# Performance work log

Hardware: AMD Instinct MI355X
Metric: run time of the kernel (lower is better)

The kernel has to match this reference:

```python
import jax, jax.numpy as jnp
import numpy as np

DIM = 1024
HEADS = 16
HEAD_DIM = DIM // HEADS
D_FF = 4 * DIM
EPS = 1e-5


def _layernorm(x, g, b):
    mu = jnp.mean(x, axis=-1, keepdims=True)
    var = jnp.mean(jnp.square(x - mu), axis=-1, keepdims=True)
    return (x - mu) * jax.lax.rsqrt(var + EPS) * g + b


def setup_inputs() -> dict:
    key = jax.random.key(0)
    ks = jax.random.split(key, 8)
    s = 0.02
    return {
        "x": jax.random.normal(ks[0], (2, 2048, DIM), dtype=jnp.float32),
        "Wqkv": jax.random.normal(ks[1], (DIM, 3 * DIM), dtype=jnp.float32) * s,
        "bqkv": jnp.zeros((3 * DIM,), dtype=jnp.float32),
        "Wout": jax.random.normal(ks[2], (DIM, DIM), dtype=jnp.float32) * s,
        "bout": jnp.zeros((DIM,), dtype=jnp.float32),
        "W1": jax.random.normal(ks[3], (DIM, D_FF), dtype=jnp.float32) * s,
        "b1": jnp.zeros((D_FF,), dtype=jnp.float32),
        "W2": jax.random.normal(ks[4], (D_FF, DIM), dtype=jnp.float32) * s,
        "b2": jnp.zeros((DIM,), dtype=jnp.float32),
        "g1": jnp.ones((DIM,), dtype=jnp.float32),
        "be1": jnp.zeros((DIM,), dtype=jnp.float32),
        "g2": jnp.ones((DIM,), dtype=jnp.float32),
        "be2": jnp.zeros((DIM,), dtype=jnp.float32),
    }


def reference(x, Wqkv, bqkv, Wout, bout, W1, b1, W2, b2, g1, be1, g2, be2):
    B, T, C = x.shape
    # --- multi-head self-attention (explicit QK^T softmax, no mask/cache) ---
    qkv = (x @ Wqkv + bqkv).reshape(B, T, 3, HEADS, HEAD_DIM)
    q = qkv[:, :, 0].transpose(0, 2, 1, 3)  # (B,H,T,hd)
    k = qkv[:, :, 1].transpose(0, 2, 1, 3)
    v = qkv[:, :, 2].transpose(0, 2, 1, 3)
    scale = HEAD_DIM ** -0.5
    scores = jnp.einsum("bhqd,bhkd->bhqk", q, k) * scale  # (B,H,T,T)
    attn = jax.nn.softmax(scores, axis=-1)
    o = jnp.einsum("bhqk,bhkd->bhqd", attn, v)
    o = o.transpose(0, 2, 1, 3).reshape(B, T, C)
    attn_out = o @ Wout + bout
    # --- Post-LN: LN applied to sublayer output, then residual ---
    x = x + _layernorm(attn_out, g1, be1)
    # --- FFN with exact GELU ---
    h = jax.nn.gelu(x @ W1 + b1, approximate=False)
    ffn_out = h @ W2 + b2
    x = x + _layernorm(ffn_out, g2, be2)
    return x
```

## Files before the change

### kernel.cpp

```cpp
#include <hip/hip_runtime.h>
#include <cstdint>
#include <cstddef>

#define DIM 1024
#define HEADS 16
#define HD 64
#define DFF 4096
#define TSEQ 2048
#define EPS 1e-5f

#define WAITCNT_VM4 0xF74
#define WAITCNT_VM0 0xF70
#define WAITCNT_VM8 0xF78
#define WAITCNT_VM4_LGKM0 0x074
#define WAITCNT_VM0_LGKM0 0x070

typedef __bf16 bf16x8 __attribute__((ext_vector_type(8)));
typedef float floatx4 __attribute__((ext_vector_type(4)));

__device__ __forceinline__ unsigned short f2bf(float f) {
  union { float f; unsigned int u; } v; v.f = f;
  return (unsigned short)((v.u + 0x7FFFu + ((v.u >> 16) & 1u)) >> 16);
}

__device__ __forceinline__ float gelu_f(float v) {
  const float u = v * (0.7978845608f + 0.0356774081f * v * v);
  const float e = __expf(2.0f * u);
  const float t = 1.0f - 2.0f / (e + 1.0f);
  return 0.5f * v * (1.0f + t);
}

__device__ __forceinline__ void async16(const void* g, void* l) {
  __builtin_amdgcn_global_load_lds(
      (const __attribute__((address_space(1))) void*)g,
      (__attribute__((address_space(3))) void*)l, 16, 0, 0);
}

__global__ __launch_bounds__(256) void prep_all(const float* __restrict__ x,
                                                const float* __restrict__ Wqkv,
                                                const float* __restrict__ Wout,
                                                const float* __restrict__ W1,
                                                const float* __restrict__ W2,
                                                unsigned short* __restrict__ xb,
                                                unsigned short* __restrict__ WqkvT,
                                                unsigned short* __restrict__ WoutT,
                                                unsigned short* __restrict__ W1T,
                                                unsigned short* __restrict__ W2T) {
  const int bid = blockIdx.x;
  const int tid = threadIdx.x;
  if (bid < 4096) {
    const int i = bid * 256 + tid;
    float4 v = ((const float4*)x)[i];
    ushort4 o;
    o.x = f2bf(v.x); o.y = f2bf(v.y); o.z = f2bf(v.z); o.w = f2bf(v.w);
    ((ushort4*)xb)[i] = o;
    return;
  }
  int id = bid - 4096;
  const float* src; unsigned short* dst; int R, C, gx;
  if (id < 3072)      {            src = Wqkv; dst = WqkvT; R = 1024; C = 3072; gx = 96; }
  else if (id < 4096) { id -= 3072; src = Wout; dst = WoutT; R = 1024; C = 1024; gx = 32; }
  else if (id < 8192) { id -= 4096; src = W1;   dst = W1T;   R = 1024; C = 4096; gx = 128; }
  else                { id -= 8192; src = W2;   dst = W2T;   R = 4096; C = 1024; gx = 32; }
  const int c0 = (id % gx) * 32, r0 = (id / gx) * 32;
  const int tx = tid & 31, ty = tid >> 5;
  __shared__ float tile[32][33];
#pragma unroll
  for (int i = 0; i < 32; i += 8)
    tile[ty + i][tx] = src[(size_t)(r0 + ty + i) * C + c0 + tx];
  __syncthreads();
#pragma unroll
  for (int i = 0; i < 32; i += 8)
    dst[(size_t)(c0 + ty + i) * R + r0 + tx] = f2bf(tile[tx][ty + i]);
}

#define PIPELINED_KLOOP(NIT, STRIDE_EXPR)                                           \
  auto issue = [&](int s, int k0) {                                                  \
    async16(Ab0 + k0, &lds[s][tid * 8]);                                             \
    async16(Ab1 + k0, &lds[s][2048 + tid * 8]);                                      \
    async16(Bb0 + k0, &lds[s][4096 + tid * 8]);                                      \
    async16(Bb1 + k0, &lds[s][6144 + tid * 8]);                                      \
  };                                                                                 \
  issue(0, 0);                                                                       \
  issue(1, 32);                                                                      \
  int sidx = 0;                                                                      \
  for (int k = 0; k < (NIT); k++) {                                                  \
    if (k < (NIT)-1) __builtin_amdgcn_s_waitcnt(WAITCNT_VM4);                        \
    else             __builtin_amdgcn_s_waitcnt(WAITCNT_VM0);                        \
    __builtin_amdgcn_s_barrier();                                                    \
    if (k + 2 < (NIT)) {                                                             \
      int s2 = sidx + 2; if (s2 >= 3) s2 -= 3;                                       \
      issue(s2, (k + 2) * 32);                                                       \
    }                                                                                \
    bf16x8 af[4], bg[4];                                                             \
    _Pragma("unroll")                                                                \
    for (int mi = 0; mi < 4; mi++)                                                   \
      af[mi] = *(const bf16x8*)&lds[sidx][(wm + mi * 16 + l16) * 32 + quad * 8];     \
    _Pragma("unroll")                                                                \
    for (int ni = 0; ni < 4; ni++)                                                   \
      bg[ni] = *(const bf16x8*)&lds[sidx][4096 + (wn + ni * 16 + l16) * 32 + quad * 8]; \
    _Pragma("unroll")                                                                \
    for (int mi = 0; mi < 4; mi++)                                                   \
      _Pragma("unroll")                                                              \
      for (int ni = 0; ni < 4; ni++)                                                 \
        acc[mi][ni] =                                                                \
            __builtin_amdgcn_mfma_f32_16x16x32_bf16(af[mi], bg[ni], acc[mi][ni], 0, 0, 0); \
    sidx = (sidx == 2) ? 0 : sidx + 1;                                               \
  }

template <int EPI>
__global__ __launch_bounds__(256) void gemm_bt(const unsigned short* __restrict__ A,
                                               const unsigned short* __restrict__ Bt,
                                               const float* __restrict__ bias,
                                               void* __restrict__ Cout,
                                               int M, int N, int K) {
  __shared__ unsigned short lds[3][8192];
  const int tid = threadIdx.x;
  const int bm = blockIdx.y * 128, bn = blockIdx.x * 128;
  const int wave = tid >> 6, lane = tid & 63;
  const int l16 = lane & 15, quad = lane >> 4;
  const int wm = (wave >> 1) * 64, wn = (wave & 1) * 64;

  floatx4 acc[4][4] = {};

  const int srow = tid >> 2;
  const int scol = (tid & 3) * 8;

  const unsigned short* Ab0 = A + (size_t)(bm + srow) * K + scol;
  const unsigned short* Ab1 = A + (size_t)(bm + 64 + srow) * K + scol;
  const unsigned short* Bb0 = Bt + (size_t)(bn + srow) * K + scol;
  const unsigned short* Bb1 = Bt + (size_t)(bn + 64 + srow) * K + scol;

  const int nit = K >> 5;
  PIPELINED_KLOOP(nit, 32)
  __syncthreads();

  if (EPI == 0) {
#pragma unroll
    for (int ni = 0; ni < 4; ni++) {
      const int col = bn + wn + ni * 16 + l16;
      const float bv = bias[col];
#pragma unroll
      for (int mi = 0; mi < 4; mi++) {
        const int row0 = bm + wm + mi * 16 + quad * 4;
#pragma unroll
        for (int r = 0; r < 4; r++)
          ((float*)Cout)[(size_t)(row0 + r) * N + col] = acc[mi][ni][r] + bv;
      }
    }
  } else {
    unsigned short* eb = &lds[0][wave * 1152];
    float bvv[4];
#pragma unroll
    for (int ni = 0; ni < 4; ni++) bvv[ni] = bias[bn + wn + ni * 16 + l16];
    const int lrow = lane >> 2, ck = lane & 3;
#pragma unroll
    for (int mi = 0; mi < 4; mi++) {
#pragma unroll
      for (int ni = 0; ni < 4; ni++)
#pragma unroll
        for (int r = 0; r < 4; r++)
          eb[(quad * 4 + r) * 72 + ni * 16 + l16] =
              f2bf(gelu_f(acc[mi][ni][r] + bvv[ni]));
      __syncthreads();
      unsigned short* gp =
          (unsigned short*)Cout + (size_t)(bm + wm + mi * 16 + lrow) * N + bn + wn;
#pragma unroll
      for (int j = 0; j < 2; j++)
        *(uint4*)(gp + j * 32 + ck * 8) = *(const uint4*)&eb[lrow * 72 + j * 32 + ck * 8];
      __syncthreads();
    }
  }
}

__global__ __launch_bounds__(256) void gemm_splitk(const unsigned short* __restrict__ A,
                                                   const unsigned short* __restrict__ Bt,
                                                   float* __restrict__ Cp,
                                                   int M, int N, int Ktot, int Ksl) {
  __shared__ unsigned short lds[3][8192];
  const int tid = threadIdx.x;
  const int bm = blockIdx.y * 128, bn = blockIdx.x * 128;
  const int koff = blockIdx.z * Ksl;
  const int wave = tid >> 6, lane = tid & 63;
  const int l16 = lane & 15, quad = lane >> 4;
  const int wm = (wave >> 1) * 64, wn = (wave & 1) * 64;

  floatx4 acc[4][4] = {};

  const int srow = tid >> 2;
  const int scol = (tid & 3) * 8;

  const unsigned short* Ab0 = A + (size_t)(bm + srow) * Ktot + koff + scol;
  const unsigned short* Ab1 = A + (size_t)(bm + 64 + srow) * Ktot + koff + scol;
  const unsigned short* Bb0 = Bt + (size_t)(bn + srow) * Ktot + koff + scol;
  const unsigned short* Bb1 = Bt + (size_t)(bn + 64 + srow) * Ktot + koff + scol;

  const int nit = Ksl >> 5;
  PIPELINED_KLOOP(nit, 32)

  float* out = Cp + (size_t)blockIdx.z * M * (size_t)N;
#pragma unroll
  for (int ni = 0; ni < 4; ni++) {
    const int col = bn + wn + ni * 16 + l16;
#pragma unroll
    for (int mi = 0; mi < 4; mi++) {
      const int row0 = bm + wm + mi * 16 + quad * 4;
#pragma unroll
      for (int r = 0; r < 4; r++)
        out[(size_t)(row0 + r) * N + col] = acc[mi][ni][r];
    }
  }
}

__global__ __launch_bounds__(256) void gemm_qkv(const unsigned short* __restrict__ A,
                                                const unsigned short* __restrict__ Bt,
                                                const float* __restrict__ bias,
                                                unsigned short* __restrict__ Qg,
                                                unsigned short* __restrict__ Kg,
                                                unsigned short* __restrict__ Vtg) {
  const int K = 1024;
  __shared__ unsigned short lds[3][8192];
  const int tid = threadIdx.x;
  const int bm = blockIdx.y * 128, bn = blockIdx.x * 128;
  const int wave = tid >> 6, lane = tid & 63;
  const int l16 = lane & 15, quad = lane >> 4;
  const int wm = (wave >> 1) * 64, wn = (wave & 1) * 64;

  floatx4 acc[4][4] = {};

  const int srow = tid >> 2;
  const int scol = (tid & 3) * 8;

  const unsigned short* Ab0 = A + (size_t)(bm + srow) * K + scol;
  const unsigned short* Ab1 = A + (size_t)(bm + 64 + srow) * K + scol;
  const unsigned short* Bb0 = Bt + (size_t)(bn + srow) * K + scol;
  const unsigned short* Bb1 = Bt + (size_t)(bn + 64 + srow) * K + scol;

  const int nit = K >> 5;
  PIPELINED_KLOOP(nit, 32)

#pragma unroll
  for (int ni = 0; ni < 4; ni++) {
    const int col = bn + wn + ni * 16 + l16;
    const float bv = bias[col];
    const int sec = col >> 10;
    const int cc = col & 1023;
    const int hh = cc >> 6, dd = cc & 63;
#pragma unroll
    for (int mi = 0; mi < 4; mi++) {
      const int row0 = bm + wm + mi * 16 + quad * 4;
      const int b2 = row0 >> 11, tt0 = row0 & 2047;
      if (sec == 0) {
        unsigned short* q = Qg + ((size_t)(b2 * HEADS + hh) * TSEQ + tt0) * HD + dd;
#pragma unroll
        for (int r = 0; r < 4; r++)
          q[(size_t)r * HD] = f2bf((acc[mi][ni][r] + bv) * 0.125f);
      } else if (sec == 1) {
        unsigned short* k = Kg + ((size_t)(b2 * HEADS + hh) * TSEQ + tt0) * HD + dd;
#pragma unroll
        for (int r = 0; r < 4; r++)
          k[(size_t)r * HD] = f2bf(acc[mi][ni][r] + bv);
      } else {
        ushort4 o;
        o.x = f2bf(acc[mi][ni][0] + bv);
        o.y = f2bf(acc[mi][ni][1] + bv);
        o.z = f2bf(acc[mi][ni][2] + bv);
        o.w = f2bf(acc[mi][ni][3] + bv);
        *(ushort4*)(Vtg + ((size_t)(b2 * HEADS + hh) * HD + dd) * TSEQ + tt0) = o;
      }
    }
  }
}

__global__ __launch_bounds__(256) void attn_mfma(const unsigned short* __restrict__ Qg,
                                                 const unsigned short* __restrict__ Kg,
                                                 const unsigned short* __restrict__ Vtg,
                                                 unsigned short* __restrict__ ob) {
  __shared__ unsigned short QPs[128 * 64];
  __shared__ unsigned short Ks[3][64 * 64];
  __shared__ unsigned short Vs[3][64 * 64];
  const int qt = blockIdx.x, h = blockIdx.y, b = blockIdx.z;
  const int tid = threadIdx.x;
  const int w = tid >> 6, lane = tid & 63, l16 = lane & 15, quad = lane >> 4;

  const int r0 = tid >> 3;
  const int c0 = (tid & 7) ^ (r0 & 7);

  const char* Qbase = (const char*)(Qg + ((size_t)(b * HEADS + h) * TSEQ + qt * 128) * HD);
  const char* Kbase = (const char*)(Kg + (size_t)(b * HEADS + h) * TSEQ * HD);
  const char* Vbase = (const char*)(Vtg + (size_t)(b * HEADS + h) * HD * TSEQ);

  auto issueKV = [&](int s, int ch) {
    const size_t koff = (size_t)ch * 64;
#pragma unroll
    for (int i = 0; i < 2; i++) {
      async16(Kbase + (koff + r0 + i * 32) * 128 + c0 * 16,
              (char*)Ks[s] + (i * 256 + tid) * 16);
      async16(Vbase + (size_t)(r0 + i * 32) * (TSEQ * 2) + koff * 2 + c0 * 16,
              (char*)Vs[s] + (i * 256 + tid) * 16);
    }
  };

#pragma unroll
  for (int i = 0; i < 4; i++)
    async16(Qbase + (size_t)(r0 + i * 32) * 128 + c0 * 16, (char*)QPs + (i * 256 + tid) * 16);
  issueKV(0, 0);
  issueKV(1, 1);

  __builtin_amdgcn_s_waitcnt(WAITCNT_VM8);
  __builtin_amdgcn_s_barrier();

  bf16x8 qf[2][2];
#pragma unroll
  for (int mi = 0; mi < 2; mi++)
#pragma unroll
    for (int kt = 0; kt < 2; kt++) {
      const int row = w * 32 + mi * 16 + l16;
      qf[mi][kt] = *(const bf16x8*)((const char*)QPs + row * 128 +
                                    (((quad + 4 * kt) ^ (row & 7)) * 16));
    }

  union { unsigned short u[8]; bf16x8 b; } onesu;
#pragma unroll
  for (int j = 0; j < 8; j++) onesu.u[j] = 0x3F80;
  const bf16x8 ones = onesu.b;

  floatx4 oacc[2][5] = {};
  char* Pw = (char*)QPs + w * 4096;

  const int NC = TSEQ / 64;
  int sidx = 0;
  for (int ch = 0; ch < NC; ch++) {
    if (ch < NC - 1) __builtin_amdgcn_s_waitcnt(WAITCNT_VM4_LGKM0);
    else             __builtin_amdgcn_s_waitcnt(WAITCNT_VM0_LGKM0);
    __builtin_amdgcn_s_barrier();
    if (ch + 2 < NC) {
      int s2 = sidx + 2; if (s2 >= 3) s2 -= 3;
      issueKV(s2, ch + 2);
    }
    floatx4 sacc[2][4] = {};
#pragma unroll
    for (int kt = 0; kt < 2; kt++) {
#pragma unroll
      for (int ni = 0; ni < 4; ni++) {
        const int row = ni * 16 + l16;
        bf16x8 kf = *(const bf16x8*)((const char*)Ks[sidx] + row * 128 +
                                     (((quad + 4 * kt) ^ (row & 7)) * 16));
#pragma unroll
        for (int mi = 0; mi < 2; mi++)
          sacc[mi][ni] =
              __builtin_amdgcn_mfma_f32_16x16x32_bf16(qf[mi][kt], kf, sacc[mi][ni], 0, 0, 0);
      }
    }
#pragma unroll
    for (int mi = 0; mi < 2; mi++)
#pragma unroll
      for (int ni = 0; ni < 4; ni++)
#pragma unroll
        for (int r = 0; r < 4; r++) {
          const float p = __expf(sacc[mi][ni][r]);
          const unsigned int pu = __builtin_bit_cast(unsigned int, p);
          const int m = mi * 16 + quad * 4 + r;
          const int key = ni * 16 + l16;
          *((unsigned short*)(Pw + m * 128 + (((key >> 3) ^ (m & 7)) * 16) +
                              (key & 7) * 2)) = (unsigned short)(pu >> 16);
        }
#pragma unroll
    for (int kt = 0; kt < 2; kt++) {
      bf16x8 pf[2], vf[4];
#pragma unroll
      for (int mi = 0; mi < 2; mi++) {
        const int row = mi * 16 + l16;
        pf[mi] = *(const bf16x8*)(Pw + row * 128 + (((quad + 4 * kt) ^ (row & 7)) * 16));
      }
#pragma unroll
      for (int nj = 0; nj < 4; nj++) {
        const int vrow = nj * 16 + l16;
        vf[nj] = *(const bf16x8*)((const char*)Vs[sidx] + vrow * 128 +
                                  (((quad + 4 * kt) ^ (vrow & 7)) * 16));
      }
#pragma unroll
      for (int mi = 0; mi < 2; mi++) {
#pragma unroll
        for (int nj = 0; nj < 4; nj++)
          oacc[mi][nj] =
              __builtin_amdgcn_mfma_f32_16x16x32_bf16(pf[mi], vf[nj], oacc[mi][nj], 0, 0, 0);
        oacc[mi][4] =
            __builtin_amdgcn_mfma_f32_16x16x32_bf16(pf[mi], ones, oacc[mi][4], 0, 0, 0);
      }
    }
    sidx = (sidx == 2) ? 0 : sidx + 1;
  }

#pragma unroll
  for (int mi = 0; mi < 2; mi++)
#pragma unroll
    for (int r = 0; r < 4; r++) {
      const float inv = 1.0f / oacc[mi][4][r];
      const int t = qt * 128 + w * 32 + mi * 16 + quad * 4 + r;
      unsigned short* orow = ob + (size_t)(b * TSEQ + t) * DIM + h * HD + l16;
#pragma unroll
      for (int nj = 0; nj < 4; nj++)
        orow[nj * 16] = f2bf(oacc[mi][nj][r] * inv);
    }
}

template <int NP, int WBF>
__global__ __launch_bounds__(256) void add_ln_red(const float* __restrict__ xin,
                                                  const float* __restrict__ parts,
                                                  const float* __restrict__ bias,
                                                  const float* __restrict__ gw,
                                                  const float* __restrict__ bw,
                                                  float* __restrict__ xout,
                                                  unsigned short* __restrict__ xbf) {
  const size_t MN = (size_t)4096 * DIM;
  const int row = blockIdx.x;
  const int tid = threadIdx.x;
  const int c = tid * 4;
  const size_t base = (size_t)row * DIM;
  float4 v = *(const float4*)(parts + base + c);
#pragma unroll
  for (int p = 1; p < NP; p++) {
    float4 t = *(const float4*)(parts + p * MN + base + c);
    v.x += t.x; v.y += t.y; v.z += t.z; v.w += t.w;
  }
  float4 bb = *(const float4*)(bias + c);
  v.x += bb.x; v.y += bb.y; v.z += bb.z; v.w += bb.w;

  float s = v.x + v.y + v.z + v.w;
  float s2 = v.x * v.x + v.y * v.y + v.z * v.z + v.w * v.w;
#pragma unroll
  for (int off = 1; off < 64; off <<= 1) {
    s += __shfl_xor(s, off);
    s2 += __shfl_xor(s2, off);
  }
  __shared__ float rsum[4], rsq[4];
  if ((tid & 63) == 0) { rsum[tid >> 6] = s; rsq[tid >> 6] = s2; }
  __syncthreads();
  s = rsum[0] + rsum[1] + rsum[2] + rsum[3];
  s2 = rsq[0] + rsq[1] + rsq[2] + rsq[3];
  const float mu = s * (1.0f / DIM);
  const float var = s2 * (1.0f / DIM) - mu * mu;
  const float rstd = rsqrtf(var + EPS);
  float4 xv = *(const float4*)(xin + base + c);
  float4 gv = *(const float4*)(gw + c);
  float4 bv = *(const float4*)(bw + c);
  float4 o;
  o.x = xv.x + (v.x - mu) * rstd * gv.x + bv.x;
  o.y = xv.y + (v.y - mu) * rstd * gv.y + bv.y;
  o.z = xv.z + (v.z - mu) * rstd * gv.z + bv.z;
  o.w = xv.w + (v.w - mu) * rstd * gv.w + bv.w;
  *(float4*)(xout + base + c) = o;
  if (WBF) {
    ushort4 ob;
    ob.x = f2bf(o.x); ob.y = f2bf(o.y); ob.z = f2bf(o.z); ob.w = f2bf(o.w);
    *(ushort4*)(xbf + base + c) = ob;
  }
}

extern "C" void kernel_launch(void* const* d_in, const int* in_sizes, int n_in,
                              void* d_out, int out_size, void* d_ws, size_t ws_size,
                              hipStream_t stream) {
  const float* x    = (const float*)d_in[0];
  const float* Wqkv = (const float*)d_in[1];
  const float* bqkv = (const float*)d_in[2];
  const float* Wout = (const float*)d_in[3];
  const float* bout = (const float*)d_in[4];
  const float* W1   = (const float*)d_in[5];
  const float* b1   = (const float*)d_in[6];
  const float* W2   = (const float*)d_in[7];
  const float* b2   = (const float*)d_in[8];
  const float* g1   = (const float*)d_in[9];
  const float* be1  = (const float*)d_in[10];
  const float* g2   = (const float*)d_in[11];
  const float* be2  = (const float*)d_in[12];

  char* w = (char*)d_ws;
  const size_t MB = 1048576;
  unsigned short* xb     = (unsigned short*)(w + 0 * MB);
  unsigned short* WqkvT  = (unsigned short*)(w + 8 * MB);
  unsigned short* WoutT  = (unsigned short*)(w + 14 * MB);
  unsigned short* W1T    = (unsigned short*)(w + 16 * MB);
  unsigned short* W2T    = (unsigned short*)(w + 24 * MB);
  unsigned short* Qb     = (unsigned short*)(w + 32 * MB);
  unsigned short* Kb     = (unsigned short*)(w + 40 * MB);
  unsigned short* Vtb    = (unsigned short*)(w + 48 * MB);
  unsigned short* obuf   = (unsigned short*)(w + 64 * MB);
  float*          atno_p = (float*)(w + 72 * MB);
  float*          x1     = (float*)(w + 104 * MB);
  unsigned short* x1b    = (unsigned short*)(w + 120 * MB);
  unsigned short* hb     = (unsigned short*)(w + 128 * MB);
  float*          ffn_p  = (float*)(w + 32 * MB);

  prep_all<<<16384, 256, 0, stream>>>(x, Wqkv, Wout, W1, W2, xb, WqkvT, WoutT, W1T, W2T);

  gemm_qkv<<<dim3(24, 32), 256, 0, stream>>>(xb, WqkvT, bqkv, Qb, Kb, Vtb);
  attn_mfma<<<dim3(16, 16, 2), 256, 0, stream>>>(Qb, Kb, Vtb, obuf);
  gemm_splitk<<<dim3(8, 32, 2), 256, 0, stream>>>(obuf, WoutT, atno_p, 4096, 1024, 1024, 512);
  add_ln_red<2, 1><<<4096, 256, 0, stream>>>(x, atno_p, bout, g1, be1, x1, x1b);
  gemm_bt<1><<<dim3(32, 32), 256, 0, stream>>>(x1b, W1T, b1, hb, 4096, 4096, 1024);
  gemm_splitk<<<dim3(8, 32, 2), 256, 0, stream>>>(hb, W2T, ffn_p, 4096, 1024, 4096, 2048);
  add_ln_red<2, 0><<<4096, 256, 0, stream>>>(x1, ffn_p, b2, g2, be2, (float*)d_out, nullptr);
}
```

Baseline: 364.4 us.

## Split attention key range in two halves and add combine kernel

```diff
diff --git a/kernel.cpp b/kernel.cpp
--- a/kernel.cpp
+++ b/kernel.cpp
@@ -11,8 +11,6 @@
 
 #define WAITCNT_VM4 0xF74
 #define WAITCNT_VM0 0xF70
-#define WAITCNT_VM8 0xF78
-#define WAITCNT_VM4_LGKM0 0x074
 #define WAITCNT_VM0_LGKM0 0x070
 
 typedef __bf16 bf16x8 __attribute__((ext_vector_type(8)));
@@ -21,6 +19,14 @@
 __device__ __forceinline__ unsigned short f2bf(float f) {
   union { float f; unsigned int u; } v; v.f = f;
   return (unsigned short)((v.u + 0x7FFFu + ((v.u >> 16) & 1u)) >> 16);
+}
+
+__device__ __forceinline__ float fast_exp2(float x) {
+#if __has_builtin(__builtin_amdgcn_exp2f)
+  return __builtin_amdgcn_exp2f(x);
+#else
+  return exp2f(x);
+#endif
 }
 
 __device__ __forceinline__ float gelu_f(float v) {
@@ -254,7 +260,7 @@
         unsigned short* q = Qg + ((size_t)(b2 * HEADS + hh) * TSEQ + tt0) * HD + dd;
 #pragma unroll
         for (int r = 0; r < 4; r++)
-          q[(size_t)r * HD] = f2bf((acc[mi][ni][r] + bv) * 0.125f);
+          q[(size_t)r * HD] = f2bf((acc[mi][ni][r] + bv) * 0.1803368867f);
       } else if (sec == 1) {
         unsigned short* k = Kg + ((size_t)(b2 * HEADS + hh) * TSEQ + tt0) * HD + dd;
 #pragma unroll
@@ -275,11 +281,15 @@
 __global__ __launch_bounds__(256) void attn_mfma(const unsigned short* __restrict__ Qg,
                                                  const unsigned short* __restrict__ Kg,
                                                  const unsigned short* __restrict__ Vtg,
-                                                 unsigned short* __restrict__ ob) {
+                                                 float* __restrict__ Op,
+                                                 float* __restrict__ Lp) {
   __shared__ unsigned short QPs[128 * 64];
-  __shared__ unsigned short Ks[3][64 * 64];
-  __shared__ unsigned short Vs[3][64 * 64];
-  const int qt = blockIdx.x, h = blockIdx.y, b = blockIdx.z;
+  __shared__ unsigned short Ks[2][64 * 64];
+  __shared__ unsigned short Vs[2][64 * 64];
+  const int idx = blockIdx.x;
+  const int bh2 = idx & 63, qt = idx >> 6;
+  const int half = bh2 & 1, bh = bh2 >> 1;
+  const int h = bh & 15, b = bh >> 4;
   const int tid = threadIdx.x;
   const int w = tid >> 6, lane = tid & 63, l16 = lane & 15, quad = lane >> 4;
 
@@ -287,8 +297,10 @@
   const int c0 = (tid & 7) ^ (r0 & 7);
 
   const char* Qbase = (const char*)(Qg + ((size_t)(b * HEADS + h) * TSEQ + qt * 128) * HD);
-  const char* Kbase = (const char*)(Kg + (size_t)(b * HEADS + h) * TSEQ * HD);
-  const char* Vbase = (const char*)(Vtg + (size_t)(b * HEADS + h) * HD * TSEQ);
+  const char* Kbase = (const char*)(Kg + (size_t)(b * HEADS + h) * TSEQ * HD) +
+                      (size_t)half * 1024 * 128;
+  const char* Vbase = (const char*)(Vtg + (size_t)(b * HEADS + h) * HD * TSEQ) +
+                      (size_t)half * 2048;
 
   auto issueKV = [&](int s, int ch) {
     const size_t koff = (size_t)ch * 64;
@@ -305,9 +317,8 @@
   for (int i = 0; i < 4; i++)
     async16(Qbase + (size_t)(r0 + i * 32) * 128 + c0 * 16, (char*)QPs + (i * 256 + tid) * 16);
   issueKV(0, 0);
-  issueKV(1, 1);
-
-  __builtin_amdgcn_s_waitcnt(WAITCNT_VM8);
+
+  __builtin_amdgcn_s_waitcnt(WAITCNT_VM4);
   __builtin_amdgcn_s_barrier();
 
   bf16x8 qf[2][2];
@@ -328,23 +339,19 @@
   floatx4 oacc[2][5] = {};
   char* Pw = (char*)QPs + w * 4096;
 
-  const int NC = TSEQ / 64;
-  int sidx = 0;
+  const int NC = 16;
   for (int ch = 0; ch < NC; ch++) {
-    if (ch < NC - 1) __builtin_amdgcn_s_waitcnt(WAITCNT_VM4_LGKM0);
-    else             __builtin_amdgcn_s_waitcnt(WAITCNT_VM0_LGKM0);
+    const int s = ch & 1;
+    __builtin_amdgcn_s_waitcnt(WAITCNT_VM0_LGKM0);
     __builtin_amdgcn_s_barrier();
-    if (ch + 2 < NC) {
-      int s2 = sidx + 2; if (s2 >= 3) s2 -= 3;
-      issueKV(s2, ch + 2);
-    }
+    if (ch + 1 < NC) issueKV(s ^ 1, ch + 1);
     floatx4 sacc[2][4] = {};
 #pragma unroll
     for (int kt = 0; kt < 2; kt++) {
 #pragma unroll
       for (int ni = 0; ni < 4; ni++) {
         const int row = ni * 16 + l16;
-        bf16x8 kf = *(const bf16x8*)((const char*)Ks[sidx] + row * 128 +
+        bf16x8 kf = *(const bf16x8*)((const char*)Ks[s] + row * 128 +
                                      (((quad + 4 * kt) ^ (row & 7)) * 16));
 #pragma unroll
         for (int mi = 0; mi < 2; mi++)
@@ -358,7 +365,7 @@
       for (int ni = 0; ni < 4; ni++)
 #pragma unroll
         for (int r = 0; r < 4; r++) {
-          const float p = __expf(sacc[mi][ni][r]);
+          const float p = fast_exp2(sacc[mi][ni][r]);
           const unsigned int pu = __builtin_bit_cast(unsigned int, p);
           const int m = mi * 16 + quad * 4 + r;
           const int key = ni * 16 + l16;
@@ -376,7 +383,7 @@
 #pragma unroll
       for (int nj = 0; nj < 4; nj++) {
         const int vrow = nj * 16 + l16;
-        vf[nj] = *(const bf16x8*)((const char*)Vs[sidx] + vrow * 128 +
+        vf[nj] = *(const bf16x8*)((const char*)Vs[s] + vrow * 128 +
                                   (((quad + 4 * kt) ^ (vrow & 7)) * 16));
       }
 #pragma unroll
@@ -389,20 +396,43 @@
             __builtin_amdgcn_mfma_f32_16x16x32_bf16(pf[mi], ones, oacc[mi][4], 0, 0, 0);
       }
     }
-    sidx = (sidx == 2) ? 0 : sidx + 1;
-  }
-
+  }
+
+  float* Oh = Op + (size_t)half * (4096ull * 1024);
 #pragma unroll
   for (int mi = 0; mi < 2; mi++)
 #pragma unroll
     for (int r = 0; r < 4; r++) {
-      const float inv = 1.0f / oacc[mi][4][r];
       const int t = qt * 128 + w * 32 + mi * 16 + quad * 4 + r;
-      unsigned short* orow = ob + (size_t)(b * TSEQ + t) * DIM + h * HD + l16;
+      float* orow = Oh + ((size_t)(b * TSEQ + t)) * DIM + h * HD + l16;
 #pragma unroll
       for (int nj = 0; nj < 4; nj++)
-        orow[nj * 16] = f2bf(oacc[mi][nj][r] * inv);
-    }
+        orow[nj * 16] = oacc[mi][nj][r];
+      if (l16 == 0)
+        Lp[half * (2 * HEADS * TSEQ) + (b * HEADS + h) * TSEQ + t] = oacc[mi][4][r];
+    }
+}
+
+__global__ __launch_bounds__(256) void attn_combine(const float* __restrict__ Op,
+                                                    const float* __restrict__ Lp,
+                                                    unsigned short* __restrict__ ob) {
+  const int row = blockIdx.x;
+  const int tid = threadIdx.x;
+  const int c = tid * 4;
+  const int b = row >> 11, t = row & 2047;
+  const int hh = c >> 6;
+  const size_t MN = (size_t)4096 * DIM;
+  const int li = (b * HEADS + hh) * TSEQ + t;
+  const float l = Lp[li] + Lp[2 * HEADS * TSEQ + li];
+  const float inv = 1.0f / l;
+  float4 o1 = *(const float4*)(Op + (size_t)row * DIM + c);
+  float4 o2 = *(const float4*)(Op + MN + (size_t)row * DIM + c);
+  ushort4 o;
+  o.x = f2bf((o1.x + o2.x) * inv);
+  o.y = f2bf((o1.y + o2.y) * inv);
+  o.z = f2bf((o1.z + o2.z) * inv);
+  o.w = f2bf((o1.w + o2.w) * inv);
+  *(ushort4*)(ob + (size_t)row * DIM + c) = o;
 }
 
 template <int NP, int WBF>
@@ -486,6 +516,8 @@
   unsigned short* Kb     = (unsigned short*)(w + 40 * MB);
   unsigned short* Vtb    = (unsigned short*)(w + 48 * MB);
   unsigned short* obuf   = (unsigned short*)(w + 64 * MB);
+  float*          Opart  = (float*)(w + 72 * MB);
+  float*          Lpart  = (float*)(w + 104 * MB);
   float*          atno_p = (float*)(w + 72 * MB);
   float*          x1     = (float*)(w + 104 * MB);
   unsigned short* x1b    = (unsigned short*)(w + 120 * MB);
@@ -495,7 +527,8 @@
   prep_all<<<16384, 256, 0, stream>>>(x, Wqkv, Wout, W1, W2, xb, WqkvT, WoutT, W1T, W2T);
 
   gemm_qkv<<<dim3(24, 32), 256, 0, stream>>>(xb, WqkvT, bqkv, Qb, Kb, Vtb);
-  attn_mfma<<<dim3(16, 16, 2), 256, 0, stream>>>(Qb, Kb, Vtb, obuf);
+  attn_mfma<<<1024, 256, 0, stream>>>(Qb, Kb, Vtb, Opart, Lpart);
+  attn_combine<<<4096, 256, 0, stream>>>(Opart, Lpart, obuf);
   gemm_splitk<<<dim3(8, 32, 2), 256, 0, stream>>>(obuf, WoutT, atno_p, 4096, 1024, 1024, 512);
   add_ln_red<2, 1><<<4096, 256, 0, stream>>>(x, atno_p, bout, g1, be1, x1, x1b);
   gemm_bt<1><<<dim3(32, 32), 256, 0, stream>>>(x1b, W1T, b1, hb, 4096, 4096, 1024);
```

After: 365.9 us. Within noise of the previous version (+0.4%).

## Load K/V fragments directly from global into registers in attention, drop LDS staging

Applied to the files above, without the earlier changes.

```diff
diff --git a/kernel.cpp b/kernel.cpp
--- a/kernel.cpp
+++ b/kernel.cpp
@@ -11,9 +11,6 @@
 
 #define WAITCNT_VM4 0xF74
 #define WAITCNT_VM0 0xF70
-#define WAITCNT_VM8 0xF78
-#define WAITCNT_VM4_LGKM0 0x074
-#define WAITCNT_VM0_LGKM0 0x070
 
 typedef __bf16 bf16x8 __attribute__((ext_vector_type(8)));
 typedef float floatx4 __attribute__((ext_vector_type(4)));
@@ -21,6 +18,14 @@
 __device__ __forceinline__ unsigned short f2bf(float f) {
   union { float f; unsigned int u; } v; v.f = f;
   return (unsigned short)((v.u + 0x7FFFu + ((v.u >> 16) & 1u)) >> 16);
+}
+
+__device__ __forceinline__ float fast_exp2(float x) {
+#if __has_builtin(__builtin_amdgcn_exp2f)
+  return __builtin_amdgcn_exp2f(x);
+#else
+  return exp2f(x);
+#endif
 }
 
 __device__ __forceinline__ float gelu_f(float v) {
@@ -254,7 +259,7 @@
         unsigned short* q = Qg + ((size_t)(b2 * HEADS + hh) * TSEQ + tt0) * HD + dd;
 #pragma unroll
         for (int r = 0; r < 4; r++)
-          q[(size_t)r * HD] = f2bf((acc[mi][ni][r] + bv) * 0.125f);
+          q[(size_t)r * HD] = f2bf((acc[mi][ni][r] + bv) * 0.1803368867f);
       } else if (sec == 1) {
         unsigned short* k = Kg + ((size_t)(b2 * HEADS + hh) * TSEQ + tt0) * HD + dd;
 #pragma unroll
@@ -277,9 +282,9 @@
                                                  const unsigned short* __restrict__ Vtg,
                                                  unsigned short* __restrict__ ob) {
   __shared__ unsigned short QPs[128 * 64];
-  __shared__ unsigned short Ks[3][64 * 64];
-  __shared__ unsigned short Vs[3][64 * 64];
-  const int qt = blockIdx.x, h = blockIdx.y, b = blockIdx.z;
+  const int idx = blockIdx.x;
+  const int bh = idx & 31, qt = idx >> 5;
+  const int h = bh & 15, b = bh >> 4;
   const int tid = threadIdx.x;
   const int w = tid >> 6, lane = tid & 63, l16 = lane & 15, quad = lane >> 4;
 
@@ -287,28 +292,13 @@
   const int c0 = (tid & 7) ^ (r0 & 7);
 
   const char* Qbase = (const char*)(Qg + ((size_t)(b * HEADS + h) * TSEQ + qt * 128) * HD);
-  const char* Kbase = (const char*)(Kg + (size_t)(b * HEADS + h) * TSEQ * HD);
-  const char* Vbase = (const char*)(Vtg + (size_t)(b * HEADS + h) * HD * TSEQ);
-
-  auto issueKV = [&](int s, int ch) {
-    const size_t koff = (size_t)ch * 64;
-#pragma unroll
-    for (int i = 0; i < 2; i++) {
-      async16(Kbase + (koff + r0 + i * 32) * 128 + c0 * 16,
-              (char*)Ks[s] + (i * 256 + tid) * 16);
-      async16(Vbase + (size_t)(r0 + i * 32) * (TSEQ * 2) + koff * 2 + c0 * 16,
-              (char*)Vs[s] + (i * 256 + tid) * 16);
-    }
-  };
+  const unsigned short* Kbh = Kg + (size_t)(b * HEADS + h) * TSEQ * HD;
+  const unsigned short* Vbh = Vtg + (size_t)(b * HEADS + h) * HD * TSEQ;
 
 #pragma unroll
   for (int i = 0; i < 4; i++)
     async16(Qbase + (size_t)(r0 + i * 32) * 128 + c0 * 16, (char*)QPs + (i * 256 + tid) * 16);
-  issueKV(0, 0);
-  issueKV(1, 1);
-
-  __builtin_amdgcn_s_waitcnt(WAITCNT_VM8);
-  __builtin_amdgcn_s_barrier();
+  __syncthreads();
 
   bf16x8 qf[2][2];
 #pragma unroll
@@ -328,29 +318,40 @@
   floatx4 oacc[2][5] = {};
   char* Pw = (char*)QPs + w * 4096;
 
+  bf16x8 kf[2][4];
+#pragma unroll
+  for (int kt = 0; kt < 2; kt++)
+#pragma unroll
+    for (int ni = 0; ni < 4; ni++)
+      kf[kt][ni] =
+          *(const bf16x8*)(Kbh + (size_t)(ni * 16 + l16) * HD + (quad + 4 * kt) * 8);
+
   const int NC = TSEQ / 64;
-  int sidx = 0;
   for (int ch = 0; ch < NC; ch++) {
-    if (ch < NC - 1) __builtin_amdgcn_s_waitcnt(WAITCNT_VM4_LGKM0);
-    else             __builtin_amdgcn_s_waitcnt(WAITCNT_VM0_LGKM0);
-    __builtin_amdgcn_s_barrier();
-    if (ch + 2 < NC) {
-      int s2 = sidx + 2; if (s2 >= 3) s2 -= 3;
-      issueKV(s2, ch + 2);
-    }
+    bf16x8 vf[2][4];
+#pragma unroll
+    for (int kt = 0; kt < 2; kt++)
+#pragma unroll
+      for (int nj = 0; nj < 4; nj++)
+        vf[kt][nj] = *(const bf16x8*)(Vbh + (size_t)(nj * 16 + l16) * TSEQ + ch * 64 +
+                                      kt * 32 + quad * 8);
     floatx4 sacc[2][4] = {};
 #pragma unroll
-    for (int kt = 0; kt < 2; kt++) {
-#pragma unroll
-      for (int ni = 0; ni < 4; ni++) {
-        const int row = ni * 16 + l16;
-        bf16x8 kf = *(const bf16x8*)((const char*)Ks[sidx] + row * 128 +
-                                     (((quad + 4 * kt) ^ (row & 7)) * 16));
+    for (int kt = 0; kt < 2; kt++)
+#pragma unroll
+      for (int ni = 0; ni < 4; ni++)
 #pragma unroll
         for (int mi = 0; mi < 2; mi++)
           sacc[mi][ni] =
-              __builtin_amdgcn_mfma_f32_16x16x32_bf16(qf[mi][kt], kf, sacc[mi][ni], 0, 0, 0);
-      }
+              __builtin_amdgcn_mfma_f32_16x16x32_bf16(qf[mi][kt], kf[kt][ni], sacc[mi][ni], 0, 0, 0);
+    bf16x8 kfn[2][4];
+    if (ch + 1 < NC) {
+#pragma unroll
+      for (int kt = 0; kt < 2; kt++)
+#pragma unroll
+        for (int ni = 0; ni < 4; ni++)
+          kfn[kt][ni] = *(const bf16x8*)(Kbh + (size_t)((ch + 1) * 64 + ni * 16 + l16) * HD +
+                                         (quad + 4 * kt) * 8);
     }
 #pragma unroll
     for (int mi = 0; mi < 2; mi++)
@@ -358,7 +359,7 @@
       for (int ni = 0; ni < 4; ni++)
 #pragma unroll
         for (int r = 0; r < 4; r++) {
-          const float p = __expf(sacc[mi][ni][r]);
+          const float p = fast_exp2(sacc[mi][ni][r]);
           const unsigned int pu = __builtin_bit_cast(unsigned int, p);
           const int m = mi * 16 + quad * 4 + r;
           const int key = ni * 16 + l16;
@@ -367,29 +368,29 @@
         }
 #pragma unroll
     for (int kt = 0; kt < 2; kt++) {
-      bf16x8 pf[2], vf[4];
+      bf16x8 pf[2];
 #pragma unroll
       for (int mi = 0; mi < 2; mi++) {
         const int row = mi * 16 + l16;
         pf[mi] = *(const bf16x8*)(Pw + row * 128 + (((quad + 4 * kt) ^ (row & 7)) * 16));
       }
 #pragma unroll
-      for (int nj = 0; nj < 4; nj++) {
-        const int vrow = nj * 16 + l16;
-        vf[nj] = *(const bf16x8*)((const char*)Vs[sidx] + vrow * 128 +
-                                  (((quad + 4 * kt) ^ (vrow & 7)) * 16));
-      }
-#pragma unroll
       for (int mi = 0; mi < 2; mi++) {
 #pragma unroll
         for (int nj = 0; nj < 4; nj++)
-          oacc[mi][nj] =
-              __builtin_amdgcn_mfma_f32_16x16x32_bf16(pf[mi], vf[nj], oacc[mi][nj], 0, 0, 0);
+          oacc[mi][nj] = __builtin_amdgcn_mfma_f32_16x16x32_bf16(pf[mi], vf[kt][nj],
+                                                                 oacc[mi][nj], 0, 0, 0);
         oacc[mi][4] =
             __builtin_amdgcn_mfma_f32_16x16x32_bf16(pf[mi], ones, oacc[mi][4], 0, 0, 0);
       }
     }
-    sidx = (sidx == 2) ? 0 : sidx + 1;
+    if (ch + 1 < NC) {
+#pragma unroll
+      for (int kt = 0; kt < 2; kt++)
+#pragma unroll
+        for (int ni = 0; ni < 4; ni++)
+          kf[kt][ni] = kfn[kt][ni];
+    }
   }
 
 #pragma unroll
@@ -495,7 +496,7 @@
   prep_all<<<16384, 256, 0, stream>>>(x, Wqkv, Wout, W1, W2, xb, WqkvT, WoutT, W1T, W2T);
 
   gemm_qkv<<<dim3(24, 32), 256, 0, stream>>>(xb, WqkvT, bqkv, Qb, Kb, Vtb);
-  attn_mfma<<<dim3(16, 16, 2), 256, 0, stream>>>(Qb, Kb, Vtb, obuf);
+  attn_mfma<<<512, 256, 0, stream>>>(Qb, Kb, Vtb, obuf);
   gemm_splitk<<<dim3(8, 32, 2), 256, 0, stream>>>(obuf, WoutT, atno_p, 4096, 1024, 1024, 512);
   add_ln_red<2, 1><<<4096, 256, 0, stream>>>(x, atno_p, bout, g1, be1, x1, x1b);
   gemm_bt<1><<<dim3(32, 32), 256, 0, stream>>>(x1b, W1T, b1, hb, 4096, 4096, 1024);
```

After: 411.9 us. 13.0% more time.
